# Optimization experiments

Measured on AMD Instinct MI355X. Metric: run time of the kernel, lower is better.

## Reference

```python
import jax, jax.numpy as jnp
import numpy as np

EPS = 1e-8


def setup_inputs() -> dict:
    key = jax.random.key(0)
    k1, k2, k3 = jax.random.split(key, 3)
    B, N_in, C = 4, 49152, 64   # 12*4^6 source cells
    N_out, K = 196608, 4        # 12*4^7 target cells, 4 IDW neighbors
    x = jax.random.normal(k1, (B, N_in, C), dtype=jnp.float32)
    nn_idx = jax.random.randint(k2, (N_out, K), 0, N_in, dtype=jnp.int64)
    nn_dist = jax.random.uniform(k3, (N_out, K), dtype=jnp.float32)
    return {"x": x, "nn_idx": nn_idx, "nn_dist": nn_dist}


def reference(x, nn_idx, nn_dist):
    # Inverse-distance weights over K nearest neighbors, normalized per target cell.
    inv = 1.0 / (nn_dist + EPS)                      # [N_out, K]
    w = inv / jnp.sum(inv, axis=-1, keepdims=True)   # [N_out, K]
    gathered = x[:, nn_idx, :]                       # [B, N_out, K, C] gather along source cells
    out = jnp.einsum("bnkc,nk->bnc", gathered, w)    # weighted reduce over neighbors
    return out
```

## Files before the change

### kernel.cpp

```cpp
#include <hip/hip_runtime.h>


#define IWD_EPS 1e-8f

typedef float f32x4 __attribute__((ext_vector_type(4)));
typedef int   i32x4 __attribute__((ext_vector_type(4)));
typedef unsigned int u32x4 __attribute__((ext_vector_type(4)));
typedef unsigned int u32x2 __attribute__((ext_vector_type(2)));

__device__ __forceinline__ float bf16lo_to_f32(unsigned int v) {
    return __builtin_bit_cast(float, v << 16);
}
__device__ __forceinline__ float bf16hi_to_f32(unsigned int v) {
    return __builtin_bit_cast(float, v & 0xFFFF0000u);
}
__device__ __forceinline__ unsigned int f32_to_bf16_rne(float f) {
    unsigned int u = __builtin_bit_cast(unsigned int, f);
    u += 0x7FFFu + ((u >> 16) & 1u);
    return u >> 16;
}

__global__ __launch_bounds__(256) void iwd_convert_split_kernel(
    const float* __restrict__ x, unsigned short* __restrict__ xs, int nvec8)
{
    constexpr int N_in = 49152;
    const int i = blockIdx.x * blockDim.x + threadIdx.x;
    if (i >= nvec8) return;

    const int c    = (i * 8) & 63;
    const int rowb = (i * 8) >> 6;
    const int h    = c >> 5;
    const int c32  = c & 31;
    const int b    = rowb / N_in;
    const int row  = rowb - b * N_in;

    const f32x4 a = *reinterpret_cast<const f32x4*>(x + (size_t)i * 8);
    const f32x4 d = *reinterpret_cast<const f32x4*>(x + (size_t)i * 8 + 4);
    u32x4 p;
    p.x = f32_to_bf16_rne(a.x) | (f32_to_bf16_rne(a.y) << 16);
    p.y = f32_to_bf16_rne(a.z) | (f32_to_bf16_rne(a.w) << 16);
    p.z = f32_to_bf16_rne(d.x) | (f32_to_bf16_rne(d.y) << 16);
    p.w = f32_to_bf16_rne(d.z) | (f32_to_bf16_rne(d.w) << 16);

    unsigned short* dst = xs + (((size_t)(b * 2 + h) * N_in + row) * 32 + c32);
    __builtin_nontemporal_store(p, reinterpret_cast<u32x4*>(dst));
}

__global__ __launch_bounds__(256) void IWD_ProjLayer_65876208386401_kernel(
    const unsigned short* __restrict__ xs,
    const int*   __restrict__ nn_idx,
    const float* __restrict__ nn_dist,
    float* __restrict__ out)
{
    constexpr int N_in  = 49152;
    constexpr int N_out = 196608;

    const int bid   = blockIdx.x;
    const int xcd   = bid & 7;
    const int b     = xcd >> 1;
    const int h     = xcd & 1;
    const int chunk = bid >> 3;

    const int n   = chunk * 32 + (threadIdx.x >> 3);
    const int c32 = (threadIdx.x & 7) * 4;

    const f32x4 d4 = *reinterpret_cast<const f32x4*>(nn_dist + (size_t)n * 4);
    const i32x4 id = *reinterpret_cast<const i32x4*>(nn_idx + (size_t)n * 4);

    const float i0 = 1.0f / (d4.x + IWD_EPS);
    const float i1 = 1.0f / (d4.y + IWD_EPS);
    const float i2 = 1.0f / (d4.z + IWD_EPS);
    const float i3 = 1.0f / (d4.w + IWD_EPS);
    const float r  = 1.0f / (i0 + i1 + i2 + i3);
    const float w0 = i0 * r, w1 = i1 * r, w2 = i2 * r, w3 = i3 * r;

    const unsigned short* plane = xs + (size_t)(b * 2 + h) * N_in * 32;
    const u32x2 a0 = *reinterpret_cast<const u32x2*>(plane + id.x * 32 + c32);
    const u32x2 a1 = *reinterpret_cast<const u32x2*>(plane + id.y * 32 + c32);
    const u32x2 a2 = *reinterpret_cast<const u32x2*>(plane + id.z * 32 + c32);
    const u32x2 a3 = *reinterpret_cast<const u32x2*>(plane + id.w * 32 + c32);

    f32x4 o;
    o.x = bf16lo_to_f32(a0.x) * w0 + bf16lo_to_f32(a1.x) * w1
        + bf16lo_to_f32(a2.x) * w2 + bf16lo_to_f32(a3.x) * w3;
    o.y = bf16hi_to_f32(a0.x) * w0 + bf16hi_to_f32(a1.x) * w1
        + bf16hi_to_f32(a2.x) * w2 + bf16hi_to_f32(a3.x) * w3;
    o.z = bf16lo_to_f32(a0.y) * w0 + bf16lo_to_f32(a1.y) * w1
        + bf16lo_to_f32(a2.y) * w2 + bf16lo_to_f32(a3.y) * w3;
    o.w = bf16hi_to_f32(a0.y) * w0 + bf16hi_to_f32(a1.y) * w1
        + bf16hi_to_f32(a2.y) * w2 + bf16hi_to_f32(a3.y) * w3;

    float* op = out + ((size_t)b * N_out + n) * 64 + h * 32 + c32;
    __builtin_nontemporal_store(o, reinterpret_cast<f32x4*>(op));
}

__global__ __launch_bounds__(256) void iwd_f32_fallback_kernel(
    const float* __restrict__ x, const int* __restrict__ nn_idx,
    const float* __restrict__ nn_dist, float* __restrict__ out)
{
    constexpr int N_in = 49152, C = 64, N_out = 196608;
    const int bid = blockIdx.x, xcd = bid & 7, b = xcd >> 1;
    const int chunk = ((bid >> 3) << 1) | (xcd & 1);
    const int n  = chunk * 16 + (threadIdx.x >> 4);
    const int cq = (threadIdx.x & 15) * 4;

    const f32x4 d4 = *reinterpret_cast<const f32x4*>(nn_dist + (size_t)n * 4);
    const i32x4 id = *reinterpret_cast<const i32x4*>(nn_idx + (size_t)n * 4);
    const float i0 = 1.0f / (d4.x + IWD_EPS), i1 = 1.0f / (d4.y + IWD_EPS);
    const float i2 = 1.0f / (d4.z + IWD_EPS), i3 = 1.0f / (d4.w + IWD_EPS);
    const float r = 1.0f / (i0 + i1 + i2 + i3);
    const float w0 = i0 * r, w1 = i1 * r, w2 = i2 * r, w3 = i3 * r;

    const float* xb = x + (size_t)b * N_in * C;
    const f32x4 a0 = *reinterpret_cast<const f32x4*>(xb + (size_t)id.x * C + cq);
    const f32x4 a1 = *reinterpret_cast<const f32x4*>(xb + (size_t)id.y * C + cq);
    const f32x4 a2 = *reinterpret_cast<const f32x4*>(xb + (size_t)id.z * C + cq);
    const f32x4 a3 = *reinterpret_cast<const f32x4*>(xb + (size_t)id.w * C + cq);
    const f32x4 o = a0 * w0 + a1 * w1 + a2 * w2 + a3 * w3;
    __builtin_nontemporal_store(
        o, reinterpret_cast<f32x4*>(out + ((size_t)b * N_out + n) * C + cq));
}

extern "C" void kernel_launch(void* const* d_in, const int* in_sizes, int n_in,
                              void* d_out, int out_size, void* d_ws, size_t ws_size,
                              hipStream_t stream) {
    const float* x       = (const float*)d_in[0];
    const int*   nn_idx  = (const int*)d_in[1];
    const float* nn_dist = (const float*)d_in[2];
    float*       out     = (float*)d_out;

    constexpr int B = 4, N_in = 49152, C = 64, N_out = 196608;
    constexpr size_t XS_BYTES = (size_t)B * N_in * C * 2;

    if (ws_size >= XS_BYTES) {
        unsigned short* xs = (unsigned short*)d_ws;
        const int nvec8 = B * N_in * C / 8;
        iwd_convert_split_kernel<<<(nvec8 + 255) / 256, 256, 0, stream>>>(x, xs, nvec8);
        const int grid = (N_out / 32) * B * 2;
        IWD_ProjLayer_65876208386401_kernel<<<grid, 256, 0, stream>>>(xs, nn_idx, nn_dist, out);
    } else {
        const int grid = (N_out / 16) * B;
        iwd_f32_fallback_kernel<<<grid, 256, 0, stream>>>(x, nn_idx, nn_dist, out);
    }
}
```

Baseline: 77.12 us.

## Precompute IDW weights and offsets once, process two targets per thread

The pre-pass kernel now also computes normalized inverse-distance weights and scaled source offsets once per target cell, using fast reciprocals, and packs them into a 32-byte record in workspace. Before this, the main kernel recomputed them in each of the 8 batch/half blocks. The main gather kernel reads these records instead of nn_idx/nn_dist and handles two target cells per thread, which halves the grid and doubles the independent loads in flight. The cost is an extra 6 MB record write and read-back, more workspace, and approximate rcp in place of exact division.

```diff
diff --git a/kernel.cpp b/kernel.cpp
--- a/kernel.cpp
+++ b/kernel.cpp
@@ -20,36 +20,54 @@
     return u >> 16;
 }
 
-__global__ __launch_bounds__(256) void iwd_convert_split_kernel(
-    const float* __restrict__ x, unsigned short* __restrict__ xs, int nvec8)
+__global__ __launch_bounds__(256) void iwd_pre_kernel(
+    const float* __restrict__ x, const int* __restrict__ nn_idx,
+    const float* __restrict__ nn_dist, unsigned short* __restrict__ xs,
+    unsigned int* __restrict__ wrec, int nconvblocks, int nvec8)
 {
     constexpr int N_in = 49152;
-    const int i = blockIdx.x * blockDim.x + threadIdx.x;
-    if (i >= nvec8) return;
+    const int bid = blockIdx.x;
+    if (bid < nconvblocks) {
+        const int i = bid * 256 + threadIdx.x;
+        if (i >= nvec8) return;
+        const int c    = (i * 8) & 63;
+        const int rowb = (i * 8) >> 6;
+        const int h    = c >> 5;
+        const int c32  = c & 31;
+        const int b    = rowb / N_in;
+        const int row  = rowb - b * N_in;
 
-    const int c    = (i * 8) & 63;
-    const int rowb = (i * 8) >> 6;
-    const int h    = c >> 5;
-    const int c32  = c & 31;
-    const int b    = rowb / N_in;
-    const int row  = rowb - b * N_in;
-
-    const f32x4 a = *reinterpret_cast<const f32x4*>(x + (size_t)i * 8);
-    const f32x4 d = *reinterpret_cast<const f32x4*>(x + (size_t)i * 8 + 4);
-    u32x4 p;
-    p.x = f32_to_bf16_rne(a.x) | (f32_to_bf16_rne(a.y) << 16);
-    p.y = f32_to_bf16_rne(a.z) | (f32_to_bf16_rne(a.w) << 16);
-    p.z = f32_to_bf16_rne(d.x) | (f32_to_bf16_rne(d.y) << 16);
-    p.w = f32_to_bf16_rne(d.z) | (f32_to_bf16_rne(d.w) << 16);
-
-    unsigned short* dst = xs + (((size_t)(b * 2 + h) * N_in + row) * 32 + c32);
-    __builtin_nontemporal_store(p, reinterpret_cast<u32x4*>(dst));
+        const f32x4 a = *reinterpret_cast<const f32x4*>(x + (size_t)i * 8);
+        const f32x4 d = *reinterpret_cast<const f32x4*>(x + (size_t)i * 8 + 4);
+        u32x4 p;
+        p.x = f32_to_bf16_rne(a.x) | (f32_to_bf16_rne(a.y) << 16);
+        p.y = f32_to_bf16_rne(a.z) | (f32_to_bf16_rne(a.w) << 16);
+        p.z = f32_to_bf16_rne(d.x) | (f32_to_bf16_rne(d.y) << 16);
+        p.w = f32_to_bf16_rne(d.z) | (f32_to_bf16_rne(d.w) << 16);
+        unsigned short* dst = xs + (((size_t)(b * 2 + h) * N_in + row) * 32 + c32);
+        __builtin_nontemporal_store(p, reinterpret_cast<u32x4*>(dst));
+    } else {
+        const int n = (bid - nconvblocks) * 256 + threadIdx.x;
+        const f32x4 d4 = *reinterpret_cast<const f32x4*>(nn_dist + (size_t)n * 4);
+        const i32x4 id = *reinterpret_cast<const i32x4*>(nn_idx + (size_t)n * 4);
+        const float i0 = __builtin_amdgcn_rcpf(d4.x + IWD_EPS);
+        const float i1 = __builtin_amdgcn_rcpf(d4.y + IWD_EPS);
+        const float i2 = __builtin_amdgcn_rcpf(d4.z + IWD_EPS);
+        const float i3 = __builtin_amdgcn_rcpf(d4.w + IWD_EPS);
+        const float r  = __builtin_amdgcn_rcpf(i0 + i1 + i2 + i3);
+        f32x4 w; w.x = i0 * r; w.y = i1 * r; w.z = i2 * r; w.w = i3 * r;
+        i32x4 off; off.x = id.x * 32; off.y = id.y * 32; off.z = id.z * 32; off.w = id.w * 32;
+        unsigned int* rp = wrec + (size_t)n * 8;
+        __builtin_nontemporal_store(__builtin_bit_cast(u32x4, w),
+                                    reinterpret_cast<u32x4*>(rp));
+        __builtin_nontemporal_store(__builtin_bit_cast(u32x4, off),
+                                    reinterpret_cast<u32x4*>(rp + 4));
+    }
 }
 
 __global__ __launch_bounds__(256) void IWD_ProjLayer_65876208386401_kernel(
     const unsigned short* __restrict__ xs,
-    const int*   __restrict__ nn_idx,
-    const float* __restrict__ nn_dist,
+    const unsigned int* __restrict__ wrec,
     float* __restrict__ out)
 {
     constexpr int N_in  = 49152;
@@ -61,37 +79,49 @@
     const int h     = xcd & 1;
     const int chunk = bid >> 3;
 
-    const int n   = chunk * 32 + (threadIdx.x >> 3);
+    const int g   = threadIdx.x >> 3;
     const int c32 = (threadIdx.x & 7) * 4;
+    const int n0  = chunk * 64 + g * 2;
 
-    const f32x4 d4 = *reinterpret_cast<const f32x4*>(nn_dist + (size_t)n * 4);
-    const i32x4 id = *reinterpret_cast<const i32x4*>(nn_idx + (size_t)n * 4);
+    const unsigned int* rp = wrec + (size_t)n0 * 8;
+    const f32x4 wA = *reinterpret_cast<const f32x4*>(rp);
+    const i32x4 oA = *reinterpret_cast<const i32x4*>(rp + 4);
+    const f32x4 wB = *reinterpret_cast<const f32x4*>(rp + 8);
+    const i32x4 oB = *reinterpret_cast<const i32x4*>(rp + 12);
 
-    const float i0 = 1.0f / (d4.x + IWD_EPS);
-    const float i1 = 1.0f / (d4.y + IWD_EPS);
-    const float i2 = 1.0f / (d4.z + IWD_EPS);
-    const float i3 = 1.0f / (d4.w + IWD_EPS);
-    const float r  = 1.0f / (i0 + i1 + i2 + i3);
-    const float w0 = i0 * r, w1 = i1 * r, w2 = i2 * r, w3 = i3 * r;
+    const unsigned short* plane = xs + (size_t)(b * 2 + h) * N_in * 32 + c32;
 
-    const unsigned short* plane = xs + (size_t)(b * 2 + h) * N_in * 32;
-    const u32x2 a0 = *reinterpret_cast<const u32x2*>(plane + id.x * 32 + c32);
-    const u32x2 a1 = *reinterpret_cast<const u32x2*>(plane + id.y * 32 + c32);
-    const u32x2 a2 = *reinterpret_cast<const u32x2*>(plane + id.z * 32 + c32);
-    const u32x2 a3 = *reinterpret_cast<const u32x2*>(plane + id.w * 32 + c32);
+    const u32x2 a0 = *reinterpret_cast<const u32x2*>(plane + oA.x);
+    const u32x2 a1 = *reinterpret_cast<const u32x2*>(plane + oA.y);
+    const u32x2 a2 = *reinterpret_cast<const u32x2*>(plane + oA.z);
+    const u32x2 a3 = *reinterpret_cast<const u32x2*>(plane + oA.w);
+    const u32x2 b0 = *reinterpret_cast<const u32x2*>(plane + oB.x);
+    const u32x2 b1 = *reinterpret_cast<const u32x2*>(plane + oB.y);
+    const u32x2 b2 = *reinterpret_cast<const u32x2*>(plane + oB.z);
+    const u32x2 b3 = *reinterpret_cast<const u32x2*>(plane + oB.w);
 
-    f32x4 o;
-    o.x = bf16lo_to_f32(a0.x) * w0 + bf16lo_to_f32(a1.x) * w1
-        + bf16lo_to_f32(a2.x) * w2 + bf16lo_to_f32(a3.x) * w3;
-    o.y = bf16hi_to_f32(a0.x) * w0 + bf16hi_to_f32(a1.x) * w1
-        + bf16hi_to_f32(a2.x) * w2 + bf16hi_to_f32(a3.x) * w3;
-    o.z = bf16lo_to_f32(a0.y) * w0 + bf16lo_to_f32(a1.y) * w1
-        + bf16lo_to_f32(a2.y) * w2 + bf16lo_to_f32(a3.y) * w3;
-    o.w = bf16hi_to_f32(a0.y) * w0 + bf16hi_to_f32(a1.y) * w1
-        + bf16hi_to_f32(a2.y) * w2 + bf16hi_to_f32(a3.y) * w3;
+    f32x4 oa, ob;
+    oa.x = bf16lo_to_f32(a0.x) * wA.x + bf16lo_to_f32(a1.x) * wA.y
+         + bf16lo_to_f32(a2.x) * wA.z + bf16lo_to_f32(a3.x) * wA.w;
+    oa.y = bf16hi_to_f32(a0.x) * wA.x + bf16hi_to_f32(a1.x) * wA.y
+         + bf16hi_to_f32(a2.x) * wA.z + bf16hi_to_f32(a3.x) * wA.w;
+    oa.z = bf16lo_to_f32(a0.y) * wA.x + bf16lo_to_f32(a1.y) * wA.y
+         + bf16lo_to_f32(a2.y) * wA.z + bf16lo_to_f32(a3.y) * wA.w;
+    oa.w = bf16hi_to_f32(a0.y) * wA.x + bf16hi_to_f32(a1.y) * wA.y
+         + bf16hi_to_f32(a2.y) * wA.z + bf16hi_to_f32(a3.y) * wA.w;
 
-    float* op = out + ((size_t)b * N_out + n) * 64 + h * 32 + c32;
-    __builtin_nontemporal_store(o, reinterpret_cast<f32x4*>(op));
+    ob.x = bf16lo_to_f32(b0.x) * wB.x + bf16lo_to_f32(b1.x) * wB.y
+         + bf16lo_to_f32(b2.x) * wB.z + bf16lo_to_f32(b3.x) * wB.w;
+    ob.y = bf16hi_to_f32(b0.x) * wB.x + bf16hi_to_f32(b1.x) * wB.y
+         + bf16hi_to_f32(b2.x) * wB.z + bf16hi_to_f32(b3.x) * wB.w;
+    ob.z = bf16lo_to_f32(b0.y) * wB.x + bf16lo_to_f32(b1.y) * wB.y
+         + bf16lo_to_f32(b2.y) * wB.z + bf16lo_to_f32(b3.y) * wB.w;
+    ob.w = bf16hi_to_f32(b0.y) * wB.x + bf16hi_to_f32(b1.y) * wB.y
+         + bf16hi_to_f32(b2.y) * wB.z + bf16hi_to_f32(b3.y) * wB.w;
+
+    float* opA = out + ((size_t)b * N_out + n0) * 64 + h * 32 + c32;
+    __builtin_nontemporal_store(oa, reinterpret_cast<f32x4*>(opA));
+    __builtin_nontemporal_store(ob, reinterpret_cast<f32x4*>(opA + 64));
 }
 
 __global__ __launch_bounds__(256) void iwd_f32_fallback_kernel(
@@ -130,14 +160,21 @@
     float*       out     = (float*)d_out;
 
     constexpr int B = 4, N_in = 49152, C = 64, N_out = 196608;
-    constexpr size_t XS_BYTES = (size_t)B * N_in * C * 2;
+    constexpr size_t WREC_BYTES = (size_t)N_out * 32;
+    constexpr size_t XS_BYTES   = (size_t)B * N_in * C * 2;
 
-    if (ws_size >= XS_BYTES) {
-        unsigned short* xs = (unsigned short*)d_ws;
+    if (ws_size >= WREC_BYTES + XS_BYTES) {
+        unsigned int*   wrec = (unsigned int*)d_ws;
+        unsigned short* xs   = (unsigned short*)((char*)d_ws + WREC_BYTES);
+
         const int nvec8 = B * N_in * C / 8;
-        iwd_convert_split_kernel<<<(nvec8 + 255) / 256, 256, 0, stream>>>(x, xs, nvec8);
-        const int grid = (N_out / 32) * B * 2;
-        IWD_ProjLayer_65876208386401_kernel<<<grid, 256, 0, stream>>>(xs, nn_idx, nn_dist, out);
+        const int nconvblocks = nvec8 / 256;
+        const int nwblocks = N_out / 256;
+        iwd_pre_kernel<<<nconvblocks + nwblocks, 256, 0, stream>>>(
+            x, nn_idx, nn_dist, xs, wrec, nconvblocks, nvec8);
+
+        const int grid = (N_out / 64) * B * 2;
+        IWD_ProjLayer_65876208386401_kernel<<<grid, 256, 0, stream>>>(xs, wrec, out);
     } else {
         const int grid = (N_out / 16) * B;
         iwd_f32_fallback_kernel<<<grid, 256, 0, stream>>>(x, nn_idx, nn_dist, out);
```

Result: slower. 98.71 us (+28.0%).
